# Kernel optimization log

Measured on AMD Instinct MI355X. Metric: run time of the kernel, lower is better.

Reference implementation:

```python
import jax, jax.numpy as jnp
import numpy as np

NNODES = 8192
K = 512
NEG_SLOPE = 0.01  # torch F.leaky_relu default
EPS = 1e-12       # torch F.normalize default eps


def setup_inputs() -> dict:
    key = jax.random.key(0)
    kx, kp = jax.random.split(key)
    x = jax.random.normal(kx, (NNODES, K), dtype=jnp.float32)
    # xavier_uniform init for proto (nnodes, k)
    bound = float(np.sqrt(6.0 / (NNODES + K)))
    proto = jax.random.uniform(kp, (NNODES, K), dtype=jnp.float32,
                               minval=-bound, maxval=bound)
    return {"x": x, "proto": proto}


def reference(x, proto):
    # In-place no_grad step in torch: proto <- l2norm(proto), rows unit-norm.
    norm = jnp.sqrt(jnp.sum(proto * proto, axis=1, keepdims=True))
    pn = proto / jnp.maximum(norm, EPS)  # (nnodes, k), unit rows
    # cosine_similarity over all pairs == pn @ pn.T since rows are unit-norm.
    # This fuses torch's (nnodes, nnodes, k) broadcast into one GEMM.
    sim = jnp.einsum('ik,jk->ij', pn, pn)  # (nnodes, nnodes)
    return jnp.where(sim >= 0, sim, NEG_SLOPE * sim)
```

## Files before the change

kernel.cpp:

```cpp
#include <hip/hip_runtime.h>
#include <stdint.h>

#define NN 8192
#define KD 512
#define BM 128
#define BN 128
#define BK 32
#define NTILE (NN / BM)
#define NTRI (NTILE * (NTILE + 1) / 2)

typedef __bf16 bf16;
typedef __bf16 bf16x8 __attribute__((ext_vector_type(8)));
typedef float f32x4 __attribute__((ext_vector_type(4)));

__global__ __launch_bounds__(256) void rownorm_kernel(const float* __restrict__ proto,
                                                      bf16* __restrict__ pn) {
    const int row  = blockIdx.x * 4 + (threadIdx.x >> 6);
    const int lane = threadIdx.x & 63;
    const float4* src = (const float4*)(proto + (size_t)row * KD) + lane * 2;
    const float4 v0 = src[0];
    const float4 v1 = src[1];
    float s = v0.x*v0.x + v0.y*v0.y + v0.z*v0.z + v0.w*v0.w
            + v1.x*v1.x + v1.y*v1.y + v1.z*v1.z + v1.w*v1.w;
#pragma unroll
    for (int off = 32; off; off >>= 1) s += __shfl_xor(s, off);
    const float inv = 1.0f / fmaxf(sqrtf(s), 1e-12f);
    bf16x8 o;
    o[0] = (bf16)(v0.x*inv); o[1] = (bf16)(v0.y*inv);
    o[2] = (bf16)(v0.z*inv); o[3] = (bf16)(v0.w*inv);
    o[4] = (bf16)(v1.x*inv); o[5] = (bf16)(v1.y*inv);
    o[6] = (bf16)(v1.z*inv); o[7] = (bf16)(v1.w*inv);
    *(bf16x8*)(pn + (size_t)row * KD + lane * 8) = o;
}

__device__ __forceinline__ void gload_lds16(const bf16* g, bf16* l) {
    __builtin_amdgcn_global_load_lds(
        (const __attribute__((address_space(1))) void*)g,
        (__attribute__((address_space(3))) void*)l, 16, 0, 0);
}

__device__ __forceinline__ float lrelu(float v) {
    return (v >= 0.0f) ? v : 0.01f * v;
}

__global__ __launch_bounds__(256) void gemm_sym_kernel(const bf16* __restrict__ P,
                                                       float* __restrict__ C) {
    __shared__ bf16 sA[BM][BK];
    __shared__ bf16 sB[BN][BK];

    const int bid = blockIdx.x;
    const int swz = (bid & 7) * (NTRI / 8) + (bid >> 3);

    int tm = 0, rem = swz;
    while (rem >= NTILE - tm) { rem -= NTILE - tm; ++tm; }
    const int tn = tm + rem;

    const int tid  = threadIdx.x;
    const int w    = tid >> 6;
    const int lane = tid & 63;
    const int rowA0 = tm * BM;
    const int rowB0 = tn * BN;
    const int wm = (w >> 1) * 64;
    const int wn = (w & 1) * 64;
    const int rsel  = lane & 15;
    const int khalf = (lane >> 4) * 8;

    f32x4 acc[4][4] = {};

    for (int kt = 0; kt < KD; kt += BK) {
        if (kt) __syncthreads();
#pragma unroll
        for (int s = 0; s < 2; ++s) {
            const int chunk = (w * 2 + s) * 64 + lane;
            const int r  = chunk >> 2;
            const int ce = (chunk & 3) * 8;
            gload_lds16(P + (size_t)(rowA0 + r) * KD + kt + ce,
                        &sA[0][0] + (w * 2 + s) * 512);
            gload_lds16(P + (size_t)(rowB0 + r) * KD + kt + ce,
                        &sB[0][0] + (w * 2 + s) * 512);
        }
        __syncthreads();

        bf16x8 af[4], bfr[4];
#pragma unroll
        for (int m = 0; m < 4; ++m)
            af[m] = *(const bf16x8*)&sA[wm + m * 16 + rsel][khalf];
#pragma unroll
        for (int n = 0; n < 4; ++n)
            bfr[n] = *(const bf16x8*)&sB[wn + n * 16 + rsel][khalf];
#pragma unroll
        for (int m = 0; m < 4; ++m)
#pragma unroll
            for (int n = 0; n < 4; ++n)
                acc[m][n] = __builtin_amdgcn_mfma_f32_16x16x32_bf16(
                    af[m], bfr[n], acc[m][n], 0, 0, 0);
    }

    const int cr = (lane >> 4) * 4;
    const int cc = lane & 15;

#pragma unroll
    for (int m = 0; m < 4; ++m)
#pragma unroll
        for (int n = 0; n < 4; ++n)
#pragma unroll
            for (int r = 0; r < 4; ++r)
                C[(size_t)(rowA0 + wm + m * 16 + cr + r) * NN
                  + (rowB0 + wn + n * 16 + cc)] = lrelu(acc[m][n][r]);

    if (tm != tn) {
#pragma unroll
        for (int m = 0; m < 4; ++m)
#pragma unroll
            for (int n = 0; n < 4; ++n) {
                float4 vv;
                vv.x = lrelu(acc[m][n][0]);
                vv.y = lrelu(acc[m][n][1]);
                vv.z = lrelu(acc[m][n][2]);
                vv.w = lrelu(acc[m][n][3]);
                *(float4*)&C[(size_t)(rowB0 + wn + n * 16 + cc) * NN
                             + (rowA0 + wm + m * 16 + cr)] = vv;
            }
    }
}

extern "C" void kernel_launch(void* const* d_in, const int* in_sizes, int n_in,
                              void* d_out, int out_size, void* d_ws, size_t ws_size,
                              hipStream_t stream) {
    const float* proto = (const float*)d_in[1];
    float* C  = (float*)d_out;
    bf16* pn  = (bf16*)d_ws;

    rownorm_kernel<<<dim3(NN / 4), dim3(256), 0, stream>>>(proto, pn);
    gemm_sym_kernel<<<dim3(NTRI), dim3(256), 0, stream>>>(pn, C);
}
```

Baseline: 99.29 us.

## Pipeline GEMM K-loop with 4-stage LDS ring and async prefetch

```diff
diff --git a/kernel.cpp b/kernel.cpp
--- a/kernel.cpp
+++ b/kernel.cpp
@@ -4,10 +4,10 @@
 #define NN 8192
 #define KD 512
 #define BM 128
-#define BN 128
 #define BK 32
 #define NTILE (NN / BM)
 #define NTRI (NTILE * (NTILE + 1) / 2)
+#define NKT (KD / BK)
 
 typedef __bf16 bf16;
 typedef __bf16 bf16x8 __attribute__((ext_vector_type(8)));
@@ -43,14 +43,12 @@
     return (v >= 0.0f) ? v : 0.01f * v;
 }
 
-__global__ __launch_bounds__(256) void gemm_sym_kernel(const bf16* __restrict__ P,
-                                                       float* __restrict__ C) {
-    __shared__ bf16 sA[BM][BK];
-    __shared__ bf16 sB[BN][BK];
+__global__ __launch_bounds__(256, 2) void gemm_sym_kernel(const bf16* __restrict__ P,
+                                                          float* __restrict__ C) {
+    __shared__ bf16 sm[4][2][128 * 32];
 
     const int bid = blockIdx.x;
     const int swz = (bid & 7) * (NTRI / 8) + (bid >> 3);
-
     int tm = 0, rem = swz;
     while (rem >= NTILE - tm) { rem -= NTILE - tm; ++tm; }
     const int tn = tm + rem;
@@ -59,45 +57,72 @@
     const int w    = tid >> 6;
     const int lane = tid & 63;
     const int rowA0 = tm * BM;
-    const int rowB0 = tn * BN;
+    const int rowB0 = tn * BM;
     const int wm = (w >> 1) * 64;
     const int wn = (w & 1) * 64;
-    const int rsel  = lane & 15;
-    const int khalf = (lane >> 4) * 8;
+    const int rr = lane & 15;
+    const int h  = lane >> 4;
+
+    const bf16* gA = P + (size_t)(rowA0 + (tid >> 2)) * KD + (tid & 3) * 8;
+    const bf16* gB = P + (size_t)(rowB0 + (tid >> 2)) * KD + (tid & 3) * 8;
+    const int stL = w * 512;
+
+    const int aOff = (wm + rr) * 32 + h * 8;
+    const int bOff = (wn + rr) * 32 + h * 8;
 
     f32x4 acc[4][4] = {};
 
-    for (int kt = 0; kt < KD; kt += BK) {
-        if (kt) __syncthreads();
-#pragma unroll
-        for (int s = 0; s < 2; ++s) {
-            const int chunk = (w * 2 + s) * 64 + lane;
-            const int r  = chunk >> 2;
-            const int ce = (chunk & 3) * 8;
-            gload_lds16(P + (size_t)(rowA0 + r) * KD + kt + ce,
-                        &sA[0][0] + (w * 2 + s) * 512);
-            gload_lds16(P + (size_t)(rowB0 + r) * KD + kt + ce,
-                        &sB[0][0] + (w * 2 + s) * 512);
-        }
-        __syncthreads();
+#define VMCNT(n) asm volatile("s_waitcnt vmcnt(" #n ")" ::: "memory")
 
-        bf16x8 af[4], bfr[4];
-#pragma unroll
-        for (int m = 0; m < 4; ++m)
-            af[m] = *(const bf16x8*)&sA[wm + m * 16 + rsel][khalf];
-#pragma unroll
-        for (int n = 0; n < 4; ++n)
-            bfr[n] = *(const bf16x8*)&sB[wn + n * 16 + rsel][khalf];
-#pragma unroll
-        for (int m = 0; m < 4; ++m)
-#pragma unroll
-            for (int n = 0; n < 4; ++n)
-                acc[m][n] = __builtin_amdgcn_mfma_f32_16x16x32_bf16(
-                    af[m], bfr[n], acc[m][n], 0, 0, 0);
-    }
+#define STAGE(tt)                                                         \
+    do {                                                                  \
+        bf16* a_ = &sm[(tt) & 3][0][0];                                   \
+        bf16* b_ = &sm[(tt) & 3][1][0];                                   \
+        const int kt_ = (tt) * BK;                                        \
+        gload_lds16(gA + kt_,           a_ + stL);                        \
+        gload_lds16(gA + 64 * KD + kt_, a_ + stL + 2048);                 \
+        gload_lds16(gB + kt_,           b_ + stL);                        \
+        gload_lds16(gB + 64 * KD + kt_, b_ + stL + 2048);                 \
+    } while (0)
 
-    const int cr = (lane >> 4) * 4;
-    const int cc = lane & 15;
+#define PHASE(t, VMA)                                                     \
+    do {                                                                  \
+        const bf16* ra_ = &sm[(t) & 3][0][0];                             \
+        const bf16* rb_ = &sm[(t) & 3][1][0];                             \
+        bf16x8 af[4], bfr[4];                                             \
+        _Pragma("unroll") for (int m = 0; m < 4; ++m)                     \
+            af[m] = *(const bf16x8*)(ra_ + aOff + m * 512);               \
+        _Pragma("unroll") for (int n = 0; n < 4; ++n)                     \
+            bfr[n] = *(const bf16x8*)(rb_ + bOff + n * 512);              \
+        if ((t) + 3 < NKT) STAGE((t) + 3);                                \
+        VMA;                                                              \
+        __builtin_amdgcn_s_barrier();                                     \
+        __builtin_amdgcn_s_setprio(1);                                    \
+        _Pragma("unroll") for (int m = 0; m < 4; ++m)                     \
+            _Pragma("unroll") for (int n = 0; n < 4; ++n)                 \
+                acc[m][n] = __builtin_amdgcn_mfma_f32_16x16x32_bf16(      \
+                    af[m], bfr[n], acc[m][n], 0, 0, 0);                   \
+        __builtin_amdgcn_s_setprio(0);                                    \
+        __builtin_amdgcn_s_barrier();                                     \
+    } while (0)
+
+    STAGE(0); STAGE(1); STAGE(2);
+    VMCNT(8);
+    __builtin_amdgcn_s_barrier();
+
+    PHASE(0,  VMCNT(8));  PHASE(1,  VMCNT(8));  PHASE(2,  VMCNT(8));
+    PHASE(3,  VMCNT(8));  PHASE(4,  VMCNT(8));  PHASE(5,  VMCNT(8));
+    PHASE(6,  VMCNT(8));  PHASE(7,  VMCNT(8));  PHASE(8,  VMCNT(8));
+    PHASE(9,  VMCNT(8));  PHASE(10, VMCNT(8));  PHASE(11, VMCNT(8));
+    PHASE(12, VMCNT(8));  PHASE(13, VMCNT(4));  PHASE(14, VMCNT(0));
+    PHASE(15, (void)0);
+
+#undef PHASE
+#undef STAGE
+#undef VMCNT
+
+    const int cr = h * 4;
+    const int cc = rr;
 
 #pragma unroll
     for (int m = 0; m < 4; ++m)
```

Result: slower. 106.1 us (+6.9%).
